# Performance work log

Measured on AMD Instinct MI355X. Metric: run time of the kernel, lower is better.

Reference implementation:

```python
import math
import jax, jax.numpy as jnp
import numpy as np


def setup_inputs() -> dict:
    key = jax.random.key(0)
    k1, k2, k3, k4 = jax.random.split(key, 4)
    B, CK, CV, T, H, W = 4, 64, 512, 8, 30, 30
    mk = jax.random.normal(k1, (B, CK, T, H, W), dtype=jnp.float32)
    qk = jax.random.normal(k2, (B, CK, H, W), dtype=jnp.float32)
    mv = jax.random.normal(k3, (B, CV, T, H, W), dtype=jnp.float32)
    qv = jax.random.normal(k4, (B, CV, H, W), dtype=jnp.float32)
    return {"mk": mk, "qk": qk, "mv": mv, "qv": qv}


def reference(mk, qk, mv, qv):
    # mk: [B, CK, T, H, W], qk: [B, CK, H, W]
    # mv: [B, CV, T, H, W], qv: [B, CV, H, W]
    B, CK, T, H, W = mk.shape
    CV = mv.shape[1]
    mkf = mk.reshape(B, CK, T * H * W)          # [B, CK, THW]
    qkf = qk.reshape(B, CK, H * W)              # [B, CK, HW]
    # distance-based affinity: (2 a.b - |a|^2) / sqrt(CK)
    a_sq = jnp.sum(mkf * mkf, axis=1)[:, :, None]        # [B, THW, 1]
    ab = jnp.einsum('bcm,bcq->bmq', mkf, qkf)            # [B, THW, HW]
    affinity = (2.0 * ab - a_sq) * (1.0 / math.sqrt(CK))
    # softmax over the memory dimension (THW)
    affinity = jax.nn.softmax(affinity, axis=1)          # [B, THW, HW]
    # value readout
    mvf = mv.reshape(B, CV, T * H * W)                   # [B, CV, THW]
    mem = jnp.einsum('bcm,bmq->bcq', mvf, affinity)      # [B, CV, HW]
    mem = mem.reshape(B, CV, H, W)
    return jnp.concatenate([mem, qv], axis=1)            # [B, 2*CV, H, W]
```

## Files before the change

kernel.cpp:

```cpp
#include <hip/hip_runtime.h>

#define B_ 4
#define CK 64
#define CV 512
#define HW_ 900
#define THW 7200
#define MT 96
#define QB 64
#define CVB 128

typedef __attribute__((ext_vector_type(4))) float f32x4;
typedef __attribute__((ext_vector_type(4))) float float4_;
typedef __attribute__((ext_vector_type(8))) short s16x8;
typedef __attribute__((ext_vector_type(4))) short s16x4;

__device__ __forceinline__ short f2bf(float f) {
  union { float f; unsigned u; } x; x.f = f;
  unsigned u = x.u;
  return (short)((u + 0x7fffu + ((u >> 16) & 1u)) >> 16);
}

__global__ __launch_bounds__(256) void prep_mk_kernel(const float* __restrict__ mk,
                                                      short* __restrict__ mkT,
                                                      float* __restrict__ asq) {
  int idx = blockIdx.x * 256 + threadIdx.x;
  if (idx >= B_ * THW) return;
  int b = idx / THW, m = idx - b * THW;
  const float* src = mk + (size_t)b * CK * THW + m;
  short row[CK];
  float acc = 0.f;
#pragma unroll
  for (int k = 0; k < CK; ++k) {
    float v = src[(size_t)k * THW];
    acc += v * v;
    row[k] = f2bf(v);
  }
  short* dst = mkT + (size_t)idx * CK;
#pragma unroll
  for (int c = 0; c < CK / 8; ++c)
    *reinterpret_cast<s16x8*>(dst + c * 8) = *reinterpret_cast<s16x8*>(row + c * 8);
  asq[idx] = acc * 0.18033688011112042f;
}

__global__ __launch_bounds__(256) void prep_qk_kernel(const float* __restrict__ qk,
                                                      short* __restrict__ qkb) {
  int i = blockIdx.x * 256 + threadIdx.x;
  if (i < B_ * CK * HW_) qkb[i] = f2bf(qk[i] * 0.36067376022224085f);
}

__global__ __launch_bounds__(256) void prep_mv_kernel(const float4_* __restrict__ mv,
                                                      short* __restrict__ mvb) {
  int i = blockIdx.x * 256 + threadIdx.x;
  const int n4 = B_ * CV * THW / 4;
  if (i >= n4) return;
  float4_ v = mv[i];
  s16x4 o;
  o[0] = f2bf(v[0]); o[1] = f2bf(v[1]); o[2] = f2bf(v[2]); o[3] = f2bf(v[3]);
  *reinterpret_cast<s16x4*>(mvb + (size_t)i * 4) = o;
}

__global__ __launch_bounds__(256) void copy_qv_kernel(const float4_* __restrict__ qv,
                                                      float* __restrict__ out) {
  int i = blockIdx.x * 256 + threadIdx.x;
  const int n4 = B_ * CV * HW_ / 4;
  if (i >= n4) return;
  const int perb = CV * HW_ / 4;
  int b = i / perb, r = i - b * perb;
  float4_ v = qv[i];
  *reinterpret_cast<float4_*>(out + (size_t)b * 2 * CV * HW_ + CV * HW_ + (size_t)r * 4) = v;
}

__global__ __launch_bounds__(256, 1) void attn_kernel(const short* __restrict__ mkT,
                                                      const short* __restrict__ qkb,
                                                      const short* __restrict__ mvb,
                                                      const float* __restrict__ asq,
                                                      float* __restrict__ out) {
  __shared__ short mv_t[CVB][MT + 16];
  __shared__ short mk_t[MT][CK + 16];
  __shared__ short e_t[4][16][MT + 16];
  __shared__ float asq_t[MT];

  const int tid = threadIdx.x;
  const int wave = tid >> 6, lane = tid & 63;
  const int g = lane >> 4, c = lane & 15;
  const int qb = blockIdx.x, cvc = blockIdx.y, b = blockIdx.z;
  const int q = qb * QB + wave * 16 + c;
  const int cv0 = cvc * CVB;

  s16x8 qf[2];
  {
    const short* qs = qkb + (size_t)b * CK * HW_;
#pragma unroll
    for (int ks = 0; ks < 2; ++ks) {
#pragma unroll
      for (int j = 0; j < 8; ++j) {
        int k = ks * 32 + g * 8 + j;
        qf[ks][j] = (q < HW_) ? qs[(size_t)k * HW_ + q] : (short)0;
      }
    }
  }

  f32x4 acc[8];
#pragma unroll
  for (int i = 0; i < 8; ++i) acc[i] = (f32x4){0.f, 0.f, 0.f, 0.f};
  float denom = 0.f;

  const short* mksrc = mkT + (size_t)b * THW * CK;
  const short* mvsrc = mvb + ((size_t)b * CV + cv0) * THW;
  const float* asrc = asq + (size_t)b * THW;

  for (int it = 0; it < THW / MT; ++it) {
    const int m0 = it * MT;
    {
      const short* s0 = mksrc + (size_t)m0 * CK;
#pragma unroll
      for (int p = 0; p < 3; ++p) {
        int ch = tid + p * 256;
        int r = ch >> 3, c8 = (ch & 7) * 8;
        *reinterpret_cast<s16x8*>(&mk_t[r][c8]) =
            *reinterpret_cast<const s16x8*>(s0 + r * CK + c8);
      }
#pragma unroll
      for (int p = 0; p < 6; ++p) {
        int ch = tid + p * 256;
        int r = ch / 12, c8 = (ch % 12) * 8;
        *reinterpret_cast<s16x8*>(&mv_t[r][c8]) =
            *reinterpret_cast<const s16x8*>(mvsrc + (size_t)r * THW + m0 + c8);
      }
      if (tid < MT) asq_t[tid] = asrc[m0 + tid];
    }
    __syncthreads();

#pragma unroll
    for (int mf = 0; mf < 6; ++mf) {
      f32x4 s = (f32x4){0.f, 0.f, 0.f, 0.f};
#pragma unroll
      for (int ks = 0; ks < 2; ++ks) {
        s16x8 a = *reinterpret_cast<const s16x8*>(&mk_t[mf * 16 + c][ks * 32 + g * 8]);
        s = __builtin_amdgcn_mfma_f32_16x16x32_bf16(a, qf[ks], s, 0, 0, 0);
      }
      const int mb = mf * 16 + g * 4;
      s16x4 e4;
#pragma unroll
      for (int r = 0; r < 4; ++r) {
        float e = exp2f(s[r] - asq_t[mb + r]);
        denom += e;
        e4[r] = f2bf(e);
      }
      *reinterpret_cast<s16x4*>(&e_t[wave][c][mb]) = e4;
    }
    __syncthreads();

#pragma unroll
    for (int ks = 0; ks < 3; ++ks) {
      s16x8 bfr = *reinterpret_cast<const s16x8*>(&e_t[wave][c][ks * 32 + g * 8]);
#pragma unroll
      for (int cf = 0; cf < 8; ++cf) {
        s16x8 afr = *reinterpret_cast<const s16x8*>(&mv_t[cf * 16 + c][ks * 32 + g * 8]);
        acc[cf] = __builtin_amdgcn_mfma_f32_16x16x32_bf16(afr, bfr, acc[cf], 0, 0, 0);
      }
    }
    __syncthreads();
  }

  denom += __shfl_xor(denom, 16);
  denom += __shfl_xor(denom, 32);
  const float inv = 1.f / denom;

  if (q < HW_) {
    float* ob = out + (size_t)b * (2 * CV * HW_) + (size_t)(cv0 + g * 4) * HW_ + q;
#pragma unroll
    for (int cf = 0; cf < 8; ++cf)
#pragma unroll
      for (int r = 0; r < 4; ++r)
        ob[(size_t)(cf * 16 + r) * HW_] = acc[cf][r] * inv;
  }
}

extern "C" void kernel_launch(void* const* d_in, const int* in_sizes, int n_in,
                              void* d_out, int out_size, void* d_ws, size_t ws_size,
                              hipStream_t stream) {
  const float* mk = (const float*)d_in[0];
  const float* qk = (const float*)d_in[1];
  const float* mv = (const float*)d_in[2];
  const float* qv = (const float*)d_in[3];
  float* out = (float*)d_out;

  char* ws = (char*)d_ws;
  short* mvb = (short*)ws;
  short* mkT = (short*)(ws + 29491200);
  short* qkb = (short*)(ws + 33177600);
  float* asq = (float*)(ws + 33638400);

  prep_mk_kernel<<<dim3((B_ * THW + 255) / 256), dim3(256), 0, stream>>>(mk, mkT, asq);
  prep_qk_kernel<<<dim3((B_ * CK * HW_ + 255) / 256), dim3(256), 0, stream>>>(qk, qkb);
  prep_mv_kernel<<<dim3((B_ * CV * THW / 4 + 255) / 256), dim3(256), 0, stream>>>(
      (const float4_*)mv, mvb);
  attn_kernel<<<dim3(15, 4, B_), dim3(256), 0, stream>>>(mkT, qkb, mvb, asq, out);
  copy_qv_kernel<<<dim3((B_ * CV * HW_ / 4 + 255) / 256), dim3(256), 0, stream>>>(
      (const float4_*)qv, out);
}
```

Before: 289.4 us.

## Split memory dimension across blocks, merge prep kernels, add finalize reduction

Splits the THW reduction three ways, so the attention grid triples from 240 to 720 blocks and allows three blocks per CU via launch bounds. Each block writes partial numerators and denominators to workspace, and a new finalize kernel sums them and normalizes. The four prep/copy kernels are merged into one launch, LDS padding is reduced, and one __syncthreads is removed because each wave only reads its own e_t slice. The cost is extra partial-sum traffic through global memory and an additional kernel launch.

```diff
diff --git a/kernel.cpp b/kernel.cpp
--- a/kernel.cpp
+++ b/kernel.cpp
@@ -8,6 +8,11 @@
 #define MT 96
 #define QB 64
 #define CVB 128
+#define NS 3
+#define MSPL (THW / NS)
+#define NIT (MSPL / MT)
+#define MVP (MT + 8)
+#define MKP (CK + 8)
 
 typedef __attribute__((ext_vector_type(4))) float f32x4;
 typedef __attribute__((ext_vector_type(4))) float float4_;
@@ -20,70 +25,73 @@
   return (short)((u + 0x7fffu + ((u >> 16) & 1u)) >> 16);
 }
 
-__global__ __launch_bounds__(256) void prep_mk_kernel(const float* __restrict__ mk,
-                                                      short* __restrict__ mkT,
-                                                      float* __restrict__ asq) {
-  int idx = blockIdx.x * 256 + threadIdx.x;
-  if (idx >= B_ * THW) return;
-  int b = idx / THW, m = idx - b * THW;
-  const float* src = mk + (size_t)b * CK * THW + m;
-  short row[CK];
-  float acc = 0.f;
-#pragma unroll
-  for (int k = 0; k < CK; ++k) {
-    float v = src[(size_t)k * THW];
-    acc += v * v;
-    row[k] = f2bf(v);
+#define NBLK_A 113
+#define NBLK_B 900
+#define NBLK_C 14400
+#define NBLK_D 1800
+__global__ __launch_bounds__(256) void prep_kernel(const float* __restrict__ mk,
+                                                   const float* __restrict__ qk,
+                                                   const float* __restrict__ mv,
+                                                   const float* __restrict__ qv,
+                                                   short* __restrict__ mkT,
+                                                   short* __restrict__ qkb,
+                                                   short* __restrict__ mvb,
+                                                   float* __restrict__ asq,
+                                                   float* __restrict__ out) {
+  int bid = blockIdx.x;
+  if (bid < NBLK_A) {
+    int idx = bid * 256 + threadIdx.x;
+    if (idx >= B_ * THW) return;
+    int b = idx / THW, m = idx - b * THW;
+    const float* src = mk + (size_t)b * CK * THW + m;
+    short row[CK];
+    float acc = 0.f;
+#pragma unroll
+    for (int k = 0; k < CK; ++k) {
+      float v = src[(size_t)k * THW];
+      acc += v * v;
+      row[k] = f2bf(v);
+    }
+    short* dst = mkT + (size_t)idx * CK;
+#pragma unroll
+    for (int c = 0; c < CK / 8; ++c)
+      *reinterpret_cast<s16x8*>(dst + c * 8) = *reinterpret_cast<s16x8*>(row + c * 8);
+    asq[idx] = acc * 0.18033688011112042f;
+  } else if (bid < NBLK_A + NBLK_B) {
+    int i = (bid - NBLK_A) * 256 + threadIdx.x;
+    if (i < B_ * CK * HW_) qkb[i] = f2bf(qk[i] * 0.36067376022224085f);
+  } else if (bid < NBLK_A + NBLK_B + NBLK_C) {
+    int i = (bid - (NBLK_A + NBLK_B)) * 256 + threadIdx.x;
+    float4_ v = reinterpret_cast<const float4_*>(mv)[i];
+    s16x4 o;
+    o[0] = f2bf(v[0]); o[1] = f2bf(v[1]); o[2] = f2bf(v[2]); o[3] = f2bf(v[3]);
+    *reinterpret_cast<s16x4*>(mvb + (size_t)i * 4) = o;
+  } else {
+    int i = (bid - (NBLK_A + NBLK_B + NBLK_C)) * 256 + threadIdx.x;
+    const int perb = CV * HW_ / 4;
+    int b = i / perb, r = i - b * perb;
+    float4_ v = reinterpret_cast<const float4_*>(qv)[i];
+    *reinterpret_cast<float4_*>(out + (size_t)b * 2 * CV * HW_ + CV * HW_ + (size_t)r * 4) = v;
   }
-  short* dst = mkT + (size_t)idx * CK;
-#pragma unroll
-  for (int c = 0; c < CK / 8; ++c)
-    *reinterpret_cast<s16x8*>(dst + c * 8) = *reinterpret_cast<s16x8*>(row + c * 8);
-  asq[idx] = acc * 0.18033688011112042f;
-}
-
-__global__ __launch_bounds__(256) void prep_qk_kernel(const float* __restrict__ qk,
-                                                      short* __restrict__ qkb) {
-  int i = blockIdx.x * 256 + threadIdx.x;
-  if (i < B_ * CK * HW_) qkb[i] = f2bf(qk[i] * 0.36067376022224085f);
-}
-
-__global__ __launch_bounds__(256) void prep_mv_kernel(const float4_* __restrict__ mv,
-                                                      short* __restrict__ mvb) {
-  int i = blockIdx.x * 256 + threadIdx.x;
-  const int n4 = B_ * CV * THW / 4;
-  if (i >= n4) return;
-  float4_ v = mv[i];
-  s16x4 o;
-  o[0] = f2bf(v[0]); o[1] = f2bf(v[1]); o[2] = f2bf(v[2]); o[3] = f2bf(v[3]);
-  *reinterpret_cast<s16x4*>(mvb + (size_t)i * 4) = o;
-}
-
-__global__ __launch_bounds__(256) void copy_qv_kernel(const float4_* __restrict__ qv,
-                                                      float* __restrict__ out) {
-  int i = blockIdx.x * 256 + threadIdx.x;
-  const int n4 = B_ * CV * HW_ / 4;
-  if (i >= n4) return;
-  const int perb = CV * HW_ / 4;
-  int b = i / perb, r = i - b * perb;
-  float4_ v = qv[i];
-  *reinterpret_cast<float4_*>(out + (size_t)b * 2 * CV * HW_ + CV * HW_ + (size_t)r * 4) = v;
-}
-
-__global__ __launch_bounds__(256, 1) void attn_kernel(const short* __restrict__ mkT,
+}
+
+__global__ __launch_bounds__(256, 3) void attn_kernel(const short* __restrict__ mkT,
                                                       const short* __restrict__ qkb,
                                                       const short* __restrict__ mvb,
                                                       const float* __restrict__ asq,
-                                                      float* __restrict__ out) {
-  __shared__ short mv_t[CVB][MT + 16];
-  __shared__ short mk_t[MT][CK + 16];
-  __shared__ short e_t[4][16][MT + 16];
+                                                      float* __restrict__ part,
+                                                      float* __restrict__ denomp) {
+  __shared__ short mv_t[CVB][MVP];
+  __shared__ short mk_t[MT][MKP];
+  __shared__ short e_t[4][16][MVP];
   __shared__ float asq_t[MT];
 
   const int tid = threadIdx.x;
   const int wave = tid >> 6, lane = tid & 63;
   const int g = lane >> 4, c = lane & 15;
-  const int qb = blockIdx.x, cvc = blockIdx.y, b = blockIdx.z;
+  const int qb = blockIdx.x;
+  const int cvc = blockIdx.y & 3, s = blockIdx.y >> 2;
+  const int b = blockIdx.z;
   const int q = qb * QB + wave * 16 + c;
   const int cv0 = cvc * CVB;
 
@@ -91,13 +99,10 @@
   {
     const short* qs = qkb + (size_t)b * CK * HW_;
 #pragma unroll
-    for (int ks = 0; ks < 2; ++ks) {
-#pragma unroll
-      for (int j = 0; j < 8; ++j) {
-        int k = ks * 32 + g * 8 + j;
-        qf[ks][j] = (q < HW_) ? qs[(size_t)k * HW_ + q] : (short)0;
-      }
-    }
+    for (int ks = 0; ks < 2; ++ks)
+#pragma unroll
+      for (int j = 0; j < 8; ++j)
+        qf[ks][j] = (q < HW_) ? qs[(size_t)(ks * 32 + g * 8 + j) * HW_ + q] : (short)0;
   }
 
   f32x4 acc[8];
@@ -109,8 +114,8 @@
   const short* mvsrc = mvb + ((size_t)b * CV + cv0) * THW;
   const float* asrc = asq + (size_t)b * THW;
 
-  for (int it = 0; it < THW / MT; ++it) {
-    const int m0 = it * MT;
+  for (int it = 0; it < NIT; ++it) {
+    const int m0 = s * MSPL + it * MT;
     {
       const short* s0 = mksrc + (size_t)m0 * CK;
 #pragma unroll
@@ -133,23 +138,22 @@
 
 #pragma unroll
     for (int mf = 0; mf < 6; ++mf) {
-      f32x4 s = (f32x4){0.f, 0.f, 0.f, 0.f};
+      f32x4 sa = (f32x4){0.f, 0.f, 0.f, 0.f};
 #pragma unroll
       for (int ks = 0; ks < 2; ++ks) {
         s16x8 a = *reinterpret_cast<const s16x8*>(&mk_t[mf * 16 + c][ks * 32 + g * 8]);
-        s = __builtin_amdgcn_mfma_f32_16x16x32_bf16(a, qf[ks], s, 0, 0, 0);
+        sa = __builtin_amdgcn_mfma_f32_16x16x32_bf16(a, qf[ks], sa, 0, 0, 0);
       }
       const int mb = mf * 16 + g * 4;
       s16x4 e4;
 #pragma unroll
       for (int r = 0; r < 4; ++r) {
-        float e = exp2f(s[r] - asq_t[mb + r]);
+        float e = exp2f(sa[r] - asq_t[mb + r]);
         denom += e;
         e4[r] = f2bf(e);
       }
       *reinterpret_cast<s16x4*>(&e_t[wave][c][mb]) = e4;
     }
-    __syncthreads();
 
 #pragma unroll
     for (int ks = 0; ks < 3; ++ks) {
@@ -165,16 +169,45 @@
 
   denom += __shfl_xor(denom, 16);
   denom += __shfl_xor(denom, 32);
-  const float inv = 1.f / denom;
-
-  if (q < HW_) {
-    float* ob = out + (size_t)b * (2 * CV * HW_) + (size_t)(cv0 + g * 4) * HW_ + q;
-#pragma unroll
-    for (int cf = 0; cf < 8; ++cf)
-#pragma unroll
-      for (int r = 0; r < 4; ++r)
-        ob[(size_t)(cf * 16 + r) * HW_] = acc[cf][r] * inv;
-  }
+  if (cvc == 0 && lane < 16)
+    denomp[((size_t)s * B_ + b) * 960 + qb * QB + wave * 16 + lane] = denom;
+
+  float* pb = part + (size_t)(((s * B_ + b) * 4 + cvc) * 15 + qb) * 8192 + wave * 16 + c;
+#pragma unroll
+  for (int cf = 0; cf < 8; ++cf)
+#pragma unroll
+    for (int r = 0; r < 4; ++r)
+      pb[(size_t)(cf * 16 + g * 4 + r) * 64] = acc[cf][r];
+}
+
+__global__ __launch_bounds__(256) void finalize_kernel(const float* __restrict__ part,
+                                                       const float* __restrict__ denomp,
+                                                       float* __restrict__ out) {
+  int t = blockIdx.x * 256 + threadIdx.x;
+  int q4 = t & 15;
+  int cvl = (t >> 4) & 127;
+  int r1 = t >> 11;
+  int qb = r1 % 15;
+  int r2 = r1 / 15;
+  int cvc = r2 & 3;
+  int b = r2 >> 2;
+  int q0 = qb * QB + q4 * 4;
+  if (q0 >= HW_) return;
+  const size_t sstr = (size_t)B_ * 4 * 15 * 8192;
+  size_t base = (size_t)((b * 4 + cvc) * 15 + qb) * 8192 + cvl * 64 + q4 * 4;
+  f32x4 p = *reinterpret_cast<const f32x4*>(part + base);
+  f32x4 p1 = *reinterpret_cast<const f32x4*>(part + base + sstr);
+  f32x4 p2 = *reinterpret_cast<const f32x4*>(part + base + 2 * sstr);
+  p = p + p1 + p2;
+  const float* dp = denomp + (size_t)b * 960 + q0;
+  f32x4 d = *reinterpret_cast<const f32x4*>(dp) +
+            *reinterpret_cast<const f32x4*>(dp + B_ * 960) +
+            *reinterpret_cast<const f32x4*>(dp + 2 * B_ * 960);
+  f32x4 o;
+#pragma unroll
+  for (int j = 0; j < 4; ++j) o[j] = p[j] / d[j];
+  *reinterpret_cast<f32x4*>(out + (size_t)b * 2 * CV * HW_ +
+                            (size_t)(cvc * CVB + cvl) * HW_ + q0) = o;
 }
 
 extern "C" void kernel_launch(void* const* d_in, const int* in_sizes, int n_in,
@@ -187,16 +220,15 @@
   float* out = (float*)d_out;
 
   char* ws = (char*)d_ws;
-  short* mvb = (short*)ws;
-  short* mkT = (short*)(ws + 29491200);
-  short* qkb = (short*)(ws + 33177600);
-  float* asq = (float*)(ws + 33638400);
-
-  prep_mk_kernel<<<dim3((B_ * THW + 255) / 256), dim3(256), 0, stream>>>(mk, mkT, asq);
-  prep_qk_kernel<<<dim3((B_ * CK * HW_ + 255) / 256), dim3(256), 0, stream>>>(qk, qkb);
-  prep_mv_kernel<<<dim3((B_ * CV * THW / 4 + 255) / 256), dim3(256), 0, stream>>>(
-      (const float4_*)mv, mvb);
-  attn_kernel<<<dim3(15, 4, B_), dim3(256), 0, stream>>>(mkT, qkb, mvb, asq, out);
-  copy_qv_kernel<<<dim3((B_ * CV * HW_ / 4 + 255) / 256), dim3(256), 0, stream>>>(
-      (const float4_*)qv, out);
-}
+  short* mvb   = (short*)ws;
+  short* mkT   = (short*)(ws + 29491200);
+  short* qkb   = (short*)(ws + 33177600);
+  float* asq   = (float*)(ws + 33638400);
+  float* denomp= (float*)(ws + 33753600);
+  float* part  = (float*)(ws + 33799680);
+
+  prep_kernel<<<dim3(NBLK_A + NBLK_B + NBLK_C + NBLK_D), dim3(256), 0, stream>>>(
+      mk, qk, mv, qv, mkT, qkb, mvb, asq, out);
+  attn_kernel<<<dim3(15, 4 * NS, B_), dim3(256), 0, stream>>>(mkT, qkb, mvb, asq, part, denomp);
+  finalize_kernel<<<dim3(1920), dim3(256), 0, stream>>>(part, denomp, out);
+}
```

Measured after the change: 237.2 us. 1.22x faster.
